# Optimization experiments

Measured on AMD Instinct MI355X. Metric: run time of the kernel, lower is better.

## Reference

```python
import jax, jax.numpy as jnp
import numpy as np

B, L, D, N = 16, 512, 768, 8192


def setup_inputs() -> dict:
    key = jax.random.key(0)
    k = jax.random.split(key, 5)
    return {
        "y": jax.random.normal(k[0], (B, L, D), dtype=jnp.float32),
        "Wy_w": jax.random.normal(k[1], (D, D), dtype=jnp.float32) * 0.02,
        "Wy_b": jnp.zeros((D,), dtype=jnp.float32),
        "Wz_w": jax.random.normal(k[2], (D, D), dtype=jnp.float32) * 0.02,
        "Wz_b": jnp.zeros((D,), dtype=jnp.float32),
        "dic_z": jax.random.normal(k[3], (N, D), dtype=jnp.float32),
        "prior": jax.random.uniform(k[4], (N,), dtype=jnp.float32),
    }


def reference(y, Wy_w, Wy_b, Wz_w, Wz_b, dic_z, prior):
    # y: [B,L,D]; dic_z: [N,D]; prior: [N]
    d = y.shape[-1]
    qy = jnp.einsum('bld,ed->ble', y, Wy_w) + Wy_b          # Wy(y): [B,L,D]
    kz = jnp.einsum('nd,ed->ne', dic_z, Wz_w) + Wz_b        # Wz(dic_z): [N,D]
    scores = jnp.einsum('bld,nd->bln', qy, kz) / jnp.sqrt(jnp.float32(d))
    attn = jax.nn.softmax(scores, axis=-1)                   # [B,L,N]
    # z[b,l,d] = sum_n prior[n] * attn[b,l,n] * dic_z[n,d]
    # == (attn * prior) @ dic_z, avoiding the [L,N,D] intermediate.
    z = jnp.einsum('bln,nd->bld', attn * prior, dic_z)       # [B,L,D]
    return z
```

## Files before the change

### kernel.cpp

```cpp
#include <hip/hip_runtime.h>
#include <stdint.h>

#define M_ 8192
#define D_ 768
#define N_ 8192

typedef unsigned short u16;
typedef __attribute__((ext_vector_type(8))) unsigned short us8;
typedef __attribute__((ext_vector_type(8))) __bf16 bf16x8;
typedef __attribute__((ext_vector_type(4))) float f32x4;

__device__ __forceinline__ u16 f2bf(float f) {
  uint32_t u = __builtin_bit_cast(uint32_t, f);
  u += 0x7FFFu + ((u >> 16) & 1u);
  return (u16)(u >> 16);
}
__device__ __forceinline__ float bf2f(u16 u) {
  return __builtin_bit_cast(float, ((uint32_t)u) << 16);
}

__device__ __forceinline__ void gload_lds16(const void* g, void* l) {
  __builtin_amdgcn_global_load_lds(
      (__attribute__((address_space(1))) void*)g,
      (__attribute__((address_space(3))) void*)l, 16, 0, 0);
}

__global__ __launch_bounds__(256)
void k_cvt_bf16(const float* __restrict__ in, u16* __restrict__ out, int n4) {
  int stride = gridDim.x * blockDim.x;
  for (int i = blockIdx.x * blockDim.x + threadIdx.x; i < n4; i += stride) {
    float4 v = reinterpret_cast<const float4*>(in)[i];
    ushort4 o;
    o.x = f2bf(v.x); o.y = f2bf(v.y); o.z = f2bf(v.z); o.w = f2bf(v.w);
    reinterpret_cast<ushort4*>(out)[i] = o;
  }
}

__global__ __launch_bounds__(256)
void k_build_vt(const float* __restrict__ dic, const float* __restrict__ prior,
                u16* __restrict__ Vt) {
  __shared__ float t[32][33];
  const int n0 = blockIdx.x * 32, d0 = blockIdx.y * 32;
  const int tx = threadIdx.x, ty = threadIdx.y;
  #pragma unroll
  for (int i = ty; i < 32; i += 8)
    t[i][tx] = dic[(size_t)(n0 + i) * D_ + d0 + tx] * prior[n0 + i];
  __syncthreads();
  #pragma unroll
  for (int i = ty; i < 32; i += 8)
    Vt[(size_t)(d0 + i) * N_ + n0 + tx] = f2bf(t[tx][i]);
}

template<int EP>
__global__ __launch_bounds__(512, 2)
void k_gemm8(const u16* __restrict__ A, const u16* __restrict__ Bm,
             u16* __restrict__ Cb, float* __restrict__ Cf, float scale,
             long ldk, int K, int Ncols, int nbx, int tps, long partStride) {
  extern __shared__ u16 ldsu[];
  const int tid = threadIdx.x;
  const int lane = tid & 63, wid = tid >> 6;
  const int wr = wid >> 2, wc = wid & 3;
  const int L15 = lane & 15, L7 = lane & 7, g = lane >> 4;

  const int nwg = gridDim.x;
  const int bid = blockIdx.x;
  const int wg = ((nwg & 7) == 0) ? ((bid & 7) * (nwg >> 3) + (bid >> 3)) : bid;
  const int s = wg / tps;
  const int r = wg % tps;
  const int bx = r % nbx, by = r / nbx;
  const long m0 = (long)by * 256;
  const long n0 = (long)bx * 256;
  const int NT = K >> 6;

  int aBase[2], bBase[2];
  #pragma unroll
  for (int ks = 0; ks < 2; ++ks) {
    const int slot = (((ks * 4 + g) ^ L7) << 3);
    aBase[ks] = wr * 8192 + L15 * 64 + slot;
    bBase[ks] = 16384 + (wc >> 1) * 8192 + (wc & 1) * 4096 + L15 * 64 + slot;
  }

  const int rowoff = wid * 8 + (lane >> 3);
  const int colsw = ((lane & 7) ^ (lane >> 3)) << 3;
  const u16* Ag = A + m0 * ldk + (long)s * K;
  const u16* Bg = Bm + n0 * ldk + (long)s * K;
  u16* ldsW = ldsu + tid * 8;

  auto g1 = [&](int t, int mat, int r0) {
    if (t >= NT) return;
    const u16* src = (mat ? Bg : Ag) + (size_t)(r0 + rowoff) * ldk
                     + (size_t)t * 64 + colsw;
    gload_lds16(src, ldsW + (t & 1) * 32768 + mat * 16384 + (r0 >> 6) * 512 * 8);
  };

#define RD_B()                                                              \
  _Pragma("unroll") for (int j = 0; j < 4; ++j)                             \
    _Pragma("unroll") for (int ks = 0; ks < 2; ++ks)                        \
      bfr[j][ks] = __builtin_bit_cast(bf16x8,                               \
          *reinterpret_cast<const us8*>(&ldsu[bufOff + bBase[ks] + j * 1024]));
#define RD_A(q)                                                             \
  _Pragma("unroll") for (int t = 0; t < 2; ++t)                             \
    _Pragma("unroll") for (int ks = 0; ks < 2; ++ks)                        \
      afr[t][ks] = __builtin_bit_cast(bf16x8,                               \
          *reinterpret_cast<const us8*>(                                    \
              &ldsu[bufOff + aBase[ks] + (2 * (q) + t) * 1024]));
#define LGKM0()                                                             \
  asm volatile("s_waitcnt lgkmcnt(0)" ::: "memory");                        \
  __builtin_amdgcn_sched_barrier(0);
#define MM(p)                                                               \
  __builtin_amdgcn_s_setprio(1);                                            \
  _Pragma("unroll") for (int t = 0; t < 2; ++t)                             \
    _Pragma("unroll") for (int j = 0; j < 4; ++j)                           \
      _Pragma("unroll") for (int ks = 0; ks < 2; ++ks)                      \
        acc[2 * (p) + t][j] = __builtin_amdgcn_mfma_f32_16x16x32_bf16(      \
            afr[t][ks], bfr[j][ks], acc[2 * (p) + t][j], 0, 0, 0);          \
  __builtin_amdgcn_s_setprio(0);

  g1(0, 1, 0); g1(0, 1, 64); g1(0, 1, 128); g1(0, 1, 192);
  g1(0, 0, 0); g1(0, 0, 128); g1(0, 0, 64); g1(0, 0, 192);
  g1(1, 1, 0); g1(1, 1, 64);
  g1(1, 1, 128); g1(1, 1, 192);
  g1(1, 0, 0); g1(1, 0, 128);
  asm volatile("s_waitcnt vmcnt(6)" ::: "memory");
  __builtin_amdgcn_s_barrier();

  f32x4 acc[8][4] = {};

  for (int k = 0; k < NT; ++k) {
    const int bufOff = (k & 1) * 32768;
    bf16x8 bfr[4][2];

    {
      bf16x8 afr[2][2];
      g1(k + 1, 0, 64); g1(k + 1, 0, 192);
      RD_B(); RD_A(0);
      asm volatile("s_waitcnt lgkmcnt(8)" ::: "memory");
      __builtin_amdgcn_s_barrier();
      LGKM0();
      MM(0);
    }
    {
      bf16x8 afr[2][2];
      RD_A(1);
      g1(k + 2, 1, 0); g1(k + 2, 1, 64);
      __builtin_amdgcn_s_barrier();
      LGKM0();
      MM(1);
    }
    {
      bf16x8 afr[2][2];
      RD_A(2);
      g1(k + 2, 1, 128); g1(k + 2, 1, 192);
      __builtin_amdgcn_s_barrier();
      LGKM0();
      MM(2);
    }
    {
      bf16x8 afr[2][2];
      RD_A(3);
      g1(k + 2, 0, 0); g1(k + 2, 0, 128);
      if (k < NT - 2) asm volatile("s_waitcnt vmcnt(6)" ::: "memory");
      else            asm volatile("s_waitcnt vmcnt(0)" ::: "memory");
      __builtin_amdgcn_s_barrier();
      LGKM0();
      MM(3);
    }
  }
#undef RD_B
#undef RD_A
#undef LGKM0
#undef MM

  if (EP == 0) {
    __builtin_amdgcn_s_barrier();
    float* lsum = reinterpret_cast<float*>(ldsu);
    #pragma unroll
    for (int i = 0; i < 8; ++i) {
      #pragma unroll
      for (int q = 0; q < 4; ++q) {
        const int rl = wr * 128 + i * 16 + g * 4 + q;
        const long row = m0 + rl;
        float rsum = 0.f;
        #pragma unroll
        for (int j = 0; j < 4; ++j) {
          float v = __expf(acc[i][j][q] * scale);
          rsum += v;
          Cb[row * (long)Ncols + n0 + wc * 64 + j * 16 + L15] = f2bf(v);
        }
        lsum[rl * 68 + wc * 16 + L15] = rsum;
      }
    }
    __builtin_amdgcn_s_barrier();
    {
      const int rl = tid >> 1, half = tid & 1;
      const float4* rp =
          reinterpret_cast<const float4*>(&lsum[rl * 68 + half * 32]);
      float s4 = 0.f;
      #pragma unroll
      for (int c = 0; c < 8; ++c) {
        float4 v = rp[c];
        s4 += (v.x + v.y) + (v.z + v.w);
      }
      s4 += __shfl_xor(s4, 1);
      if (half == 0) atomicAdd(&Cf[m0 + rl], s4);
    }
  } else {
    #pragma unroll
    for (int i = 0; i < 8; ++i)
      #pragma unroll
      for (int j = 0; j < 4; ++j)
        #pragma unroll
        for (int q = 0; q < 4; ++q) {
          long row = m0 + wr * 128 + i * 16 + g * 4 + q;
          long col = n0 + wc * 64 + j * 16 + L15;
          Cf[(long)s * partStride + row * (long)Ncols + col] = acc[i][j][q];
        }
  }
}

__global__ __launch_bounds__(256)
void k_reduce2(const float* __restrict__ part, long partStride,
               const float* __restrict__ rowsum, float* __restrict__ out, int n4) {
  int stride = gridDim.x * blockDim.x;
  const float4* p0 = reinterpret_cast<const float4*>(part);
  const float4* p1 = reinterpret_cast<const float4*>(part + partStride);
  for (int i = blockIdx.x * blockDim.x + threadIdx.x; i < n4; i += stride) {
    float4 a = p0[i], b = p1[i];
    float sc = 1.0f / rowsum[(i * 4) / D_];
    float4 o;
    o.x = (a.x + b.x) * sc; o.y = (a.y + b.y) * sc;
    o.z = (a.z + b.z) * sc; o.w = (a.w + b.w) * sc;
    reinterpret_cast<float4*>(out)[i] = o;
  }
}

template<int EP>
__global__ __launch_bounds__(256, 2)
void k_gemm_nt(const u16* __restrict__ A, const u16* __restrict__ Bm,
               float* __restrict__ Cf, u16* __restrict__ Cb,
               const float* __restrict__ bias, const float* __restrict__ rowscale,
               float scale, int N, int K) {
  __shared__ u16 Al[128 * 64];
  __shared__ u16 Bl[128 * 64];
  const int tid = threadIdx.x;
  const int lane = tid & 63;
  const int wave = tid >> 6;
  const int wr = wave >> 1, wc = wave & 1;
  const long m0 = (long)blockIdx.y * 128;
  const long n0 = (long)blockIdx.x * 128;

  f32x4 acc[4][4] = {};

  const u16* gA = A + (m0 + (tid >> 3)) * (long)K + (tid & 7) * 8;
  const u16* gB = Bm + (n0 + (tid >> 3)) * (long)K + (tid & 7) * 8;

  for (int kt = 0; kt < K; kt += 64) {
    __syncthreads();
    #pragma unroll
    for (int r = 0; r < 4; ++r) {
      gload_lds16(gA + (size_t)(r * 32) * K + kt, &Al[r * 2048 + tid * 8]);
      gload_lds16(gB + (size_t)(r * 32) * K + kt, &Bl[r * 2048 + tid * 8]);
    }
    __syncthreads();
    #pragma unroll
    for (int ks = 0; ks < 2; ++ks) {
      bf16x8 av[4], bv[4];
      #pragma unroll
      for (int i = 0; i < 4; ++i) {
        av[i] = __builtin_bit_cast(bf16x8, *reinterpret_cast<const us8*>(
            &Al[(wr * 64 + i * 16 + (lane & 15)) * 64 + ks * 32 + (lane >> 4) * 8]));
        bv[i] = __builtin_bit_cast(bf16x8, *reinterpret_cast<const us8*>(
            &Bl[(wc * 64 + i * 16 + (lane & 15)) * 64 + ks * 32 + (lane >> 4) * 8]));
      }
      #pragma unroll
      for (int i = 0; i < 4; ++i)
        #pragma unroll
        for (int j = 0; j < 4; ++j)
          acc[i][j] = __builtin_amdgcn_mfma_f32_16x16x32_bf16(av[i], bv[j], acc[i][j], 0, 0, 0);
    }
  }

  #pragma unroll
  for (int i = 0; i < 4; ++i) {
    #pragma unroll
    for (int j = 0; j < 4; ++j) {
      #pragma unroll
      for (int q = 0; q < 4; ++q) {
        long row = m0 + wr * 64 + i * 16 + ((lane >> 4) * 4) + q;
        long col = n0 + wc * 64 + j * 16 + (lane & 15);
        float v = acc[i][j][q];
        if (EP == 1)      Cb[row * N + col] = f2bf(v + bias[col]);
        else if (EP == 2) Cb[row * N + col] = f2bf(v * scale);
        else              Cf[row * N + col] = v * rowscale[row];
      }
    }
  }
}

extern "C" void kernel_launch(void* const* d_in, const int* in_sizes, int n_in,
                              void* d_out, int out_size, void* d_ws, size_t ws_size,
                              hipStream_t stream) {
  (void)in_sizes; (void)n_in; (void)out_size;
  const float* y     = (const float*)d_in[0];
  const float* Wy_w  = (const float*)d_in[1];
  const float* Wy_b  = (const float*)d_in[2];
  const float* Wz_w  = (const float*)d_in[3];
  const float* Wz_b  = (const float*)d_in[4];
  const float* dic   = (const float*)d_in[5];
  const float* prior = (const float*)d_in[6];
  float* out = (float*)d_out;

  hipFuncSetAttribute(reinterpret_cast<const void*>(&k_gemm8<0>),
                      hipFuncAttributeMaxDynamicSharedMemorySize, 131072);
  hipFuncSetAttribute(reinterpret_cast<const void*>(&k_gemm8<1>),
                      hipFuncAttributeMaxDynamicSharedMemorySize, 131072);

  char* base = (char*)d_ws;
  size_t off = 0;
  auto alloc = [&](size_t bytes) -> char* {
    char* p = base + off;
    off = (off + bytes + 255) & ~(size_t)255;
    return p;
  };
  u16*  Yb   = (u16*)alloc((size_t)M_ * D_ * 2);
  u16*  Db   = (u16*)alloc((size_t)N_ * D_ * 2);
  u16*  Wyb  = (u16*)alloc((size_t)D_ * D_ * 2);
  u16*  Wzb  = (u16*)alloc((size_t)D_ * D_ * 2);
  u16*  Qb   = (u16*)alloc((size_t)M_ * D_ * 2);
  u16*  Kb   = (u16*)alloc((size_t)N_ * D_ * 2);
  u16*  Vt   = (u16*)alloc((size_t)D_ * N_ * 2);
  float* rowsum = (float*)alloc((size_t)M_ * 4);
  size_t fixed = off;
  int Mc = M_;
  while (Mc > 256 &&
         fixed + (size_t)Mc * N_ * 2 + 2 * (size_t)Mc * D_ * 4 > ws_size)
    Mc >>= 1;
  u16*   Sc   = (u16*)alloc((size_t)Mc * N_ * 2);
  float* part = (float*)alloc(2 * (size_t)Mc * D_ * 4);
  const long partStride = (long)Mc * D_;

  hipMemsetAsync(rowsum, 0, (size_t)M_ * 4, stream);

  auto cvt = [&](const float* src, u16* dst, size_t n) {
    int n4 = (int)(n / 4);
    int blocks = (n4 + 255) / 256;
    if (blocks > 2048) blocks = 2048;
    hipLaunchKernelGGL(k_cvt_bf16, dim3(blocks), dim3(256), 0, stream, src, dst, n4);
  };
  cvt(y,    Yb,  (size_t)M_ * D_);
  cvt(dic,  Db,  (size_t)N_ * D_);
  cvt(Wy_w, Wyb, (size_t)D_ * D_);
  cvt(Wz_w, Wzb, (size_t)D_ * D_);

  hipLaunchKernelGGL(k_build_vt, dim3(N_ / 32, D_ / 32), dim3(32, 8), 0, stream,
                     dic, prior, Vt);

  hipLaunchKernelGGL(HIP_KERNEL_NAME(k_gemm_nt<1>), dim3(D_ / 128, M_ / 128), dim3(256), 0, stream,
                     Yb, Wyb, (float*)nullptr, Qb, Wy_b, (const float*)nullptr, 0.f, D_, D_);
  hipLaunchKernelGGL(HIP_KERNEL_NAME(k_gemm_nt<1>), dim3(D_ / 128, N_ / 128), dim3(256), 0, stream,
                     Db, Wzb, (float*)nullptr, Kb, Wz_b, (const float*)nullptr, 0.f, D_, D_);

  const float scale = 0.036084391824351615f;
  for (int mc = 0; mc < M_; mc += Mc) {
    {
      const int nbx = N_ / 256, nby = Mc / 256;
      hipLaunchKernelGGL(HIP_KERNEL_NAME(k_gemm8<0>), dim3(nbx * nby), dim3(512), 131072, stream,
                         Qb + (size_t)mc * D_, Kb, Sc, rowsum + mc, scale,
                         (long)D_, D_, N_, nbx, nbx * nby, 0L);
    }
    {
      const int nbx = D_ / 256, nby = Mc / 256, tps = nbx * nby;
      hipLaunchKernelGGL(HIP_KERNEL_NAME(k_gemm8<1>), dim3(tps * 2), dim3(512), 131072, stream,
                         Sc, Vt, (u16*)nullptr, part, 1.0f,
                         (long)N_, N_ / 2, D_, nbx, tps, partStride);
    }
    {
      int n4 = Mc * D_ / 4;
      int blocks = (n4 + 255) / 256;
      if (blocks > 2048) blocks = 2048;
      hipLaunchKernelGGL(k_reduce2, dim3(blocks), dim3(256), 0, stream,
                         part, partStride, rowsum + mc, out + (size_t)mc * D_, n4);
    }
  }
}
```

Before: 304.9 us.

## Replace split-K attn·V GEMM and reduce pass with swizzled fused-normalize GEMM

The second GEMM (scores × prior-weighted dictionary) no longer uses the 256×256 split-K k_gemm8 kernel followed by a separate reduction. It now uses the 128×128 k_gemm_nt kernel over the full K, whose epilogue divides by the row sum and writes fp32 output directly. This removes the partial-sum buffers, their global write and read traffic, and one launch. The LDS tiles in k_gemm_nt also get an XOR swizzle to cut bank conflicts, which affects the two projection GEMMs as well. The risk is that the simpler kernel, with no double buffering and a sync on every K step, is less efficient than the tuned 8-wave kernel on this large K=8192 GEMM.

```diff
diff --git a/kernel.cpp b/kernel.cpp
--- a/kernel.cpp
+++ b/kernel.cpp
@@ -218,43 +218,30 @@
   }
 }
 
-__global__ __launch_bounds__(256)
-void k_reduce2(const float* __restrict__ part, long partStride,
-               const float* __restrict__ rowsum, float* __restrict__ out, int n4) {
-  int stride = gridDim.x * blockDim.x;
-  const float4* p0 = reinterpret_cast<const float4*>(part);
-  const float4* p1 = reinterpret_cast<const float4*>(part + partStride);
-  for (int i = blockIdx.x * blockDim.x + threadIdx.x; i < n4; i += stride) {
-    float4 a = p0[i], b = p1[i];
-    float sc = 1.0f / rowsum[(i * 4) / D_];
-    float4 o;
-    o.x = (a.x + b.x) * sc; o.y = (a.y + b.y) * sc;
-    o.z = (a.z + b.z) * sc; o.w = (a.w + b.w) * sc;
-    reinterpret_cast<float4*>(out)[i] = o;
-  }
-}
-
 template<int EP>
 __global__ __launch_bounds__(256, 2)
 void k_gemm_nt(const u16* __restrict__ A, const u16* __restrict__ Bm,
                float* __restrict__ Cf, u16* __restrict__ Cb,
-               const float* __restrict__ bias, const float* __restrict__ rowscale,
-               float scale, int N, int K) {
+               const float* __restrict__ bias, const float* __restrict__ rowsum,
+               float scale, int N, long K) {
   __shared__ u16 Al[128 * 64];
   __shared__ u16 Bl[128 * 64];
   const int tid = threadIdx.x;
   const int lane = tid & 63;
   const int wave = tid >> 6;
   const int wr = wave >> 1, wc = wave & 1;
+  const int L15 = lane & 15, L7 = lane & 7, g = lane >> 4;
   const long m0 = (long)blockIdx.y * 128;
   const long n0 = (long)blockIdx.x * 128;
 
   f32x4 acc[4][4] = {};
 
-  const u16* gA = A + (m0 + (tid >> 3)) * (long)K + (tid & 7) * 8;
-  const u16* gB = Bm + (n0 + (tid >> 3)) * (long)K + (tid & 7) * 8;
-
-  for (int kt = 0; kt < K; kt += 64) {
+  const int colsw = ((tid & 7) ^ ((tid >> 3) & 7)) * 8;
+  const u16* gA = A + (m0 + (tid >> 3)) * K + colsw;
+  const u16* gB = Bm + (n0 + (tid >> 3)) * K + colsw;
+  const int aslot = ((g) ^ L7) * 8;
+
+  for (long kt = 0; kt < K; kt += 64) {
     __syncthreads();
     #pragma unroll
     for (int r = 0; r < 4; ++r) {
@@ -264,13 +251,14 @@
     __syncthreads();
     #pragma unroll
     for (int ks = 0; ks < 2; ++ks) {
+      const int slot = ((ks * 4 + g) ^ L7) * 8;
       bf16x8 av[4], bv[4];
       #pragma unroll
       for (int i = 0; i < 4; ++i) {
         av[i] = __builtin_bit_cast(bf16x8, *reinterpret_cast<const us8*>(
-            &Al[(wr * 64 + i * 16 + (lane & 15)) * 64 + ks * 32 + (lane >> 4) * 8]));
+            &Al[(wr * 64 + i * 16 + L15) * 64 + slot]));
         bv[i] = __builtin_bit_cast(bf16x8, *reinterpret_cast<const us8*>(
-            &Bl[(wc * 64 + i * 16 + (lane & 15)) * 64 + ks * 32 + (lane >> 4) * 8]));
+            &Bl[(wc * 64 + i * 16 + L15) * 64 + slot]));
       }
       #pragma unroll
       for (int i = 0; i < 4; ++i)
@@ -279,22 +267,25 @@
           acc[i][j] = __builtin_amdgcn_mfma_f32_16x16x32_bf16(av[i], bv[j], acc[i][j], 0, 0, 0);
     }
   }
+  (void)aslot;
 
   #pragma unroll
   for (int i = 0; i < 4; ++i) {
     #pragma unroll
-    for (int j = 0; j < 4; ++j) {
-      #pragma unroll
-      for (int q = 0; q < 4; ++q) {
-        long row = m0 + wr * 64 + i * 16 + ((lane >> 4) * 4) + q;
-        long col = n0 + wc * 64 + j * 16 + (lane & 15);
+    for (int q = 0; q < 4; ++q) {
+      long row = m0 + wr * 64 + i * 16 + g * 4 + q;
+      float inv;
+      if (EP == 3) inv = 1.0f / rowsum[row];
+      #pragma unroll
+      for (int j = 0; j < 4; ++j) {
+        long col = n0 + wc * 64 + j * 16 + L15;
         float v = acc[i][j][q];
-        if (EP == 1)      Cb[row * N + col] = f2bf(v + bias[col]);
-        else if (EP == 2) Cb[row * N + col] = f2bf(v * scale);
-        else              Cf[row * N + col] = v * rowscale[row];
+        if (EP == 1) Cb[row * N + col] = f2bf(v + bias[col]);
+        else         Cf[row * N + col] = v * inv;
       }
     }
   }
+  (void)scale;
 }
 
 extern "C" void kernel_launch(void* const* d_in, const int* in_sizes, int n_in,
@@ -311,8 +302,6 @@
   float* out = (float*)d_out;
 
   hipFuncSetAttribute(reinterpret_cast<const void*>(&k_gemm8<0>),
-                      hipFuncAttributeMaxDynamicSharedMemorySize, 131072);
-  hipFuncSetAttribute(reinterpret_cast<const void*>(&k_gemm8<1>),
                       hipFuncAttributeMaxDynamicSharedMemorySize, 131072);
 
   char* base = (char*)d_ws;
@@ -332,12 +321,8 @@
   float* rowsum = (float*)alloc((size_t)M_ * 4);
   size_t fixed = off;
   int Mc = M_;
-  while (Mc > 256 &&
-         fixed + (size_t)Mc * N_ * 2 + 2 * (size_t)Mc * D_ * 4 > ws_size)
-    Mc >>= 1;
-  u16*   Sc   = (u16*)alloc((size_t)Mc * N_ * 2);
-  float* part = (float*)alloc(2 * (size_t)Mc * D_ * 4);
-  const long partStride = (long)Mc * D_;
+  while (Mc > 256 && fixed + (size_t)Mc * N_ * 2 > ws_size) Mc >>= 1;
+  u16* Sc = (u16*)alloc((size_t)Mc * N_ * 2);
 
   hipMemsetAsync(rowsum, 0, (size_t)M_ * 4, stream);
 
@@ -356,9 +341,9 @@
                      dic, prior, Vt);
 
   hipLaunchKernelGGL(HIP_KERNEL_NAME(k_gemm_nt<1>), dim3(D_ / 128, M_ / 128), dim3(256), 0, stream,
-                     Yb, Wyb, (float*)nullptr, Qb, Wy_b, (const float*)nullptr, 0.f, D_, D_);
+                     Yb, Wyb, (float*)nullptr, Qb, Wy_b, (const float*)nullptr, 0.f, D_, (long)D_);
   hipLaunchKernelGGL(HIP_KERNEL_NAME(k_gemm_nt<1>), dim3(D_ / 128, N_ / 128), dim3(256), 0, stream,
-                     Db, Wzb, (float*)nullptr, Kb, Wz_b, (const float*)nullptr, 0.f, D_, D_);
+                     Db, Wzb, (float*)nullptr, Kb, Wz_b, (const float*)nullptr, 0.f, D_, (long)D_);
 
   const float scale = 0.036084391824351615f;
   for (int mc = 0; mc < M_; mc += Mc) {
@@ -368,18 +353,8 @@
                          Qb + (size_t)mc * D_, Kb, Sc, rowsum + mc, scale,
                          (long)D_, D_, N_, nbx, nbx * nby, 0L);
     }
-    {
-      const int nbx = D_ / 256, nby = Mc / 256, tps = nbx * nby;
-      hipLaunchKernelGGL(HIP_KERNEL_NAME(k_gemm8<1>), dim3(tps * 2), dim3(512), 131072, stream,
-                         Sc, Vt, (u16*)nullptr, part, 1.0f,
-                         (long)N_, N_ / 2, D_, nbx, tps, partStride);
-    }
-    {
-      int n4 = Mc * D_ / 4;
-      int blocks = (n4 + 255) / 256;
-      if (blocks > 2048) blocks = 2048;
-      hipLaunchKernelGGL(k_reduce2, dim3(blocks), dim3(256), 0, stream,
-                         part, partStride, rowsum + mc, out + (size_t)mc * D_, n4);
-    }
-  }
-}
+    hipLaunchKernelGGL(HIP_KERNEL_NAME(k_gemm_nt<3>), dim3(D_ / 128, Mc / 128), dim3(256), 0, stream,
+                       Sc, Vt, out + (size_t)mc * D_, (u16*)nullptr,
+                       (const float*)nullptr, rowsum + mc, 0.f, D_, (long)N_);
+  }
+}
```

Measured after the change: 328.4 us. 1.08x slower.
